# Kernel tuning notes

Measured on AMD Instinct MI355X. Metric: run time of the kernel, lower is better.

Reference implementation:

```python
import jax, jax.numpy as jnp
import numpy as np

N_U, N_I, E, D = 100000, 50000, 1600000, 128


def setup_inputs() -> dict:
    key = jax.random.key(0)
    ks = jax.random.split(key, 24)
    inp = {
        "x_user": jax.random.normal(ks[0], (N_U, D), jnp.float32),
        "x_item": jax.random.normal(ks[1], (N_I, D), jnp.float32),
        "follows_src": jax.random.randint(ks[2], (E,), 0, N_U, jnp.int32),
        "follows_dst": jax.random.randint(ks[3], (E,), 0, N_U, jnp.int32),
        "rates_src": jax.random.randint(ks[4], (E,), 0, N_U, jnp.int32),
        "rates_dst": jax.random.randint(ks[5], (E,), 0, N_I, jnp.int32),
        "rev_src": jax.random.randint(ks[6], (E,), 0, N_I, jnp.int32),
        "rev_dst": jax.random.randint(ks[7], (E,), 0, N_U, jnp.int32),
    }
    scale = 1.0 / np.sqrt(D)
    wnames = ["W1_follows", "W1_rates", "W1_rev", "W2_follows", "W2_rates", "W2_rev"]
    for i, name in enumerate(wnames):
        inp[name] = jax.random.normal(ks[8 + i], (D, D), jnp.float32) * scale
    bnames = ["b1_follows", "b1_rates", "b1_rev", "b2_follows", "b2_rates", "b2_rev"]
    for i, name in enumerate(bnames):
        inp[name] = jax.random.normal(ks[14 + i], (D,), jnp.float32) * 0.02
    return inp


def _gcn_conv(x_src, src, dst, n_src, n_dst, W, b):
    """Degree-normalized GCN conv on a (possibly bipartite) relation."""
    ones = jnp.ones(src.shape, x_src.dtype)
    deg_s = jax.ops.segment_sum(ones, src, num_segments=n_src)
    deg_d = jax.ops.segment_sum(ones, dst, num_segments=n_dst)
    inv_s = jnp.where(deg_s > 0, 1.0 / jnp.sqrt(deg_s), 0.0)
    inv_d = jnp.where(deg_d > 0, 1.0 / jnp.sqrt(deg_d), 0.0)
    h = x_src @ W                                   # [n_src, out]
    norm = inv_s[src] * inv_d[dst]                  # [E]
    msg = h[src] * norm[:, None]                    # gather + scale
    out = jax.ops.segment_sum(msg, dst, num_segments=n_dst)  # scatter-add
    return out + b


def reference(x_user, x_item, follows_src, follows_dst, rates_src, rates_dst,
              rev_src, rev_dst, W1_follows, b1_follows, W1_rates, b1_rates,
              W1_rev, b1_rev, W2_follows, b2_follows, W2_rates, b2_rates,
              W2_rev, b2_rev):
    # Layer 1: HeteroConv with aggr='mean' over relations sharing dst type
    u = (_gcn_conv(x_user, follows_src, follows_dst, N_U, N_U, W1_follows, b1_follows)
         + _gcn_conv(x_item, rev_src, rev_dst, N_I, N_U, W1_rev, b1_rev)) * 0.5
    it = _gcn_conv(x_user, rates_src, rates_dst, N_U, N_I, W1_rates, b1_rates)
    u = jax.nn.relu(u)
    it = jax.nn.relu(it)
    # Layer 2 (final layer: no relu)
    u2 = (_gcn_conv(u, follows_src, follows_dst, N_U, N_U, W2_follows, b2_follows)
          + _gcn_conv(it, rev_src, rev_dst, N_I, N_U, W2_rev, b2_rev)) * 0.5
    i2 = _gcn_conv(u, rates_src, rates_dst, N_U, N_I, W2_rates, b2_rates)
    # concat node-type outputs into a single array: [N_U + N_I, D]
    return jnp.concatenate([u2, i2], axis=0)
```

## Files before the change

kernel.cpp:

```cpp
#include <hip/hip_runtime.h>
#include <math.h>

static constexpr int NU    = 100000;
static constexpr int NI    = 50000;
static constexpr int NEDGE = 1600000;
static constexpr int DIM   = 128;

static constexpr int CB  = 768;
static constexpr int GF  = (NU + 127) / 128;
static constexpr int GV  = (NI + 127) / 128;
static constexpr int FB  = 512;
static constexpr int AGU = (NU + 3) / 4;
static constexpr int AGI = (NI + 3) / 4;

__device__ __forceinline__ void count_rel(const int* __restrict__ src, const int* __restrict__ dst,
                                          int* __restrict__ deg_s, int* __restrict__ deg_d,
                                          int* __restrict__ rank, int blk, int nblk) {
  const int nchunk = NEDGE / 4;
  const int stride = nblk * 256;
  for (int c = blk * 256 + threadIdx.x; c < nchunk; c += stride) {
    int4 s = ((const int4*)src)[c];
    int4 d = ((const int4*)dst)[c];
    atomicAdd(&deg_s[s.x], 1);
    atomicAdd(&deg_s[s.y], 1);
    atomicAdd(&deg_s[s.z], 1);
    atomicAdd(&deg_s[s.w], 1);
    int4 r;
    r.x = atomicAdd(&deg_d[d.x], 1);
    r.y = atomicAdd(&deg_d[d.y], 1);
    r.z = atomicAdd(&deg_d[d.z], 1);
    r.w = atomicAdd(&deg_d[d.w], 1);
    ((int4*)rank)[c] = r;
  }
}

__device__ __forceinline__ void fill_rel(const int* __restrict__ src, const int* __restrict__ dst,
                                         const int* __restrict__ rank, const int* __restrict__ rp,
                                         int* __restrict__ csr, int blk, int nblk) {
  const int nchunk = NEDGE / 4;
  const int stride = nblk * 256;
  for (int c = blk * 256 + threadIdx.x; c < nchunk; c += stride) {
    int4 s = ((const int4*)src)[c];
    int4 d = ((const int4*)dst)[c];
    int4 r = ((const int4*)rank)[c];
    csr[rp[d.x] + r.x] = s.x;
    csr[rp[d.y] + r.y] = s.y;
    csr[rp[d.z] + r.z] = s.z;
    csr[rp[d.w] + r.w] = s.w;
  }
}

__device__ __forceinline__ void gemm_body(const float* __restrict__ A, const float* __restrict__ W,
                                          float* __restrict__ C, int M, int blk) {
  static __shared__ float As[16][132];
  static __shared__ float Bs[16][128];
  const int tid = threadIdx.x;
  const int tx = tid & 15, ty = tid >> 4;
  const int row0 = blk * 128;
  float acc[8][8];
#pragma unroll
  for (int r = 0; r < 8; ++r)
#pragma unroll
    for (int c = 0; c < 8; ++c) acc[r][c] = 0.f;

  for (int kk = 0; kk < DIM; kk += 16) {
#pragma unroll
    for (int p = 0; p < 2; ++p) {
      int r = (tid >> 2) + p * 64;
      int kc = (tid & 3) * 4;
      float4 a = make_float4(0.f, 0.f, 0.f, 0.f);
      int row = row0 + r;
      if (row < M) a = *(const float4*)(A + (size_t)row * DIM + kk + kc);
      As[kc + 0][r] = a.x; As[kc + 1][r] = a.y; As[kc + 2][r] = a.z; As[kc + 3][r] = a.w;
    }
    {
      const float4* srcp = (const float4*)(W + kk * DIM);
      float4* dstp = (float4*)(&Bs[0][0]);
      dstp[tid]       = srcp[tid];
      dstp[tid + 256] = srcp[tid + 256];
    }
    __syncthreads();
#pragma unroll
    for (int k = 0; k < 16; ++k) {
      float a[8], b[8];
      *(float4*)&a[0] = *(const float4*)&As[k][ty * 8];
      *(float4*)&a[4] = *(const float4*)&As[k][ty * 8 + 4];
      *(float4*)&b[0] = *(const float4*)&Bs[k][tx * 8];
      *(float4*)&b[4] = *(const float4*)&Bs[k][tx * 8 + 4];
#pragma unroll
      for (int r = 0; r < 8; ++r)
#pragma unroll
        for (int c = 0; c < 8; ++c) acc[r][c] += a[r] * b[c];
    }
    __syncthreads();
  }
#pragma unroll
  for (int r = 0; r < 8; ++r) {
    int row = row0 + ty * 8 + r;
    if (row < M) {
      float4* cp = (float4*)(C + (size_t)row * DIM + tx * 8);
      cp[0] = make_float4(acc[r][0], acc[r][1], acc[r][2], acc[r][3]);
      cp[1] = make_float4(acc[r][4], acc[r][5], acc[r][6], acc[r][7]);
    }
  }
}

template <int MODE, bool RELU>
__device__ __forceinline__ void agg_rows(const float* __restrict__ h, const int* __restrict__ rp,
                                         const int* __restrict__ csr, const float* __restrict__ inv_s,
                                         const float* __restrict__ inv_d, float* __restrict__ out,
                                         int n_dst, float scale, const float* __restrict__ b1,
                                         const float* __restrict__ b2, int blk) {
  const int lane = threadIdx.x & 63;
  const int row = blk * 4 + (threadIdx.x >> 6);
  if (row >= n_dst) return;
  const int e0 = rp[row], e1 = rp[row + 1];
  float ax = 0.f, ay = 0.f;
  for (int base = e0; base < e1; base += 64) {
    const int rem = e1 - base;
    const int m = rem < 64 ? rem : 64;
    int s_l = 0; float w_l = 0.f;
    if (lane < m) { s_l = csr[base + lane]; w_l = inv_s[s_l]; }
    int j = 0;
    for (; j + 3 < m; j += 4) {
      int s0 = __shfl(s_l, j), s1 = __shfl(s_l, j + 1), s2 = __shfl(s_l, j + 2), s3 = __shfl(s_l, j + 3);
      float w0 = __shfl(w_l, j), w1 = __shfl(w_l, j + 1), w2 = __shfl(w_l, j + 2), w3 = __shfl(w_l, j + 3);
      float2 v0 = ((const float2*)(h + (size_t)s0 * DIM))[lane];
      float2 v1 = ((const float2*)(h + (size_t)s1 * DIM))[lane];
      float2 v2 = ((const float2*)(h + (size_t)s2 * DIM))[lane];
      float2 v3 = ((const float2*)(h + (size_t)s3 * DIM))[lane];
      ax += w0 * v0.x + w1 * v1.x + w2 * v2.x + w3 * v3.x;
      ay += w0 * v0.y + w1 * v1.y + w2 * v2.y + w3 * v3.y;
    }
    for (; j < m; ++j) {
      int s0 = __shfl(s_l, j); float w0 = __shfl(w_l, j);
      float2 v0 = ((const float2*)(h + (size_t)s0 * DIM))[lane];
      ax += w0 * v0.x; ay += w0 * v0.y;
    }
  }
  const float invd = inv_d[row];
  float rx = ax * invd, ry = ay * invd;
  float2* op = (float2*)(out + (size_t)row * DIM);
  if (MODE == 0) {
    op[lane] = make_float2(rx, ry);
  } else {
    float bx = 0.f, by = 0.f;
    if (b1) { float2 b = ((const float2*)b1)[lane]; bx += b.x; by += b.y; }
    if (b2) { float2 b = ((const float2*)b2)[lane]; bx += b.x; by += b.y; }
    float px = 0.f, py = 0.f;
    if (MODE == 1) { float2 p = op[lane]; px = p.x; py = p.y; }
    float vx = scale * (px + rx + bx), vy = scale * (py + ry + by);
    if (RELU) { vx = fmaxf(vx, 0.f); vy = fmaxf(vy, 0.f); }
    op[lane] = make_float2(vx, vy);
  }
}

__device__ void scan_body(const int* __restrict__ deg, int n, int* __restrict__ rp) {
  static __shared__ int wsum[16];
  static __shared__ int carry_s;
  const int tid = threadIdx.x, lane = tid & 63, wid = tid >> 6;
  if (tid == 0) carry_s = 0;
  __syncthreads();
  for (int base = 0; base < n; base += 4096) {
    int i0 = base + tid * 4;
    int v0 = 0, v1 = 0, v2 = 0, v3 = 0;
    if (i0 + 3 < n) {
      int4 t = *(const int4*)(deg + i0);
      v0 = t.x; v1 = t.y; v2 = t.z; v3 = t.w;
    } else {
      if (i0     < n) v0 = deg[i0];
      if (i0 + 1 < n) v1 = deg[i0 + 1];
      if (i0 + 2 < n) v2 = deg[i0 + 2];
    }
    int s0 = v0, s1 = s0 + v1, s2 = s1 + v2, s3 = s2 + v3;
    int tot = s3;
    int x = tot;
#pragma unroll
    for (int d2 = 1; d2 < 64; d2 <<= 1) { int y = __shfl_up(x, d2); if (lane >= d2) x += y; }
    if (lane == 63) wsum[wid] = x;
    __syncthreads();
    if (wid == 0) {
      int s = (lane < 16) ? wsum[lane] : 0;
#pragma unroll
      for (int d2 = 1; d2 < 16; d2 <<= 1) { int y = __shfl_up(s, d2); if (lane >= d2) s += y; }
      if (lane < 16) wsum[lane] = s;
    }
    __syncthreads();
    int carry = carry_s;
    int woff = (wid > 0) ? wsum[wid - 1] : 0;
    int base_excl = carry + woff + (x - tot);
    if (i0     < n) rp[i0]     = base_excl;
    if (i0 + 1 < n) rp[i0 + 1] = base_excl + s0;
    if (i0 + 2 < n) rp[i0 + 2] = base_excl + s1;
    if (i0 + 3 < n) rp[i0 + 3] = base_excl + s2;
    __syncthreads();
    if (tid == 0) carry_s = carry + wsum[15];
    __syncthreads();
  }
  if (tid == 0) rp[n] = carry_s;
}


__global__ __launch_bounds__(256) void k1_kernel(
    const int* f_src, const int* f_dst, int* deg_fs, int* deg_fd, int* rank_f,
    const int* r_src, const int* r_dst, int* deg_rs, int* deg_rd, int* rank_r,
    const int* v_src, const int* v_dst, int* deg_vs, int* deg_vd, int* rank_v,
    const float* x_user, const float* x_item,
    const float* W1f, const float* W1v, const float* W1r,
    float* h_f, float* h_v, float* h_r) {
  int b = blockIdx.x;
  if (b < CB) {
    count_rel(f_src, f_dst, deg_fs, deg_fd, rank_f, b, CB);
    count_rel(r_src, r_dst, deg_rs, deg_rd, rank_r, b, CB);
    count_rel(v_src, v_dst, deg_vs, deg_vd, rank_v, b, CB);
  } else if (b < CB + GF) {
    gemm_body(x_user, W1f, h_f, NU, b - CB);
  } else if (b < CB + GF + GV) {
    gemm_body(x_item, W1v, h_v, NI, b - CB - GF);
  } else {
    gemm_body(x_user, W1r, h_r, NU, b - CB - GF - GV);
  }
}

__global__ __launch_bounds__(1024) void scan3_kernel(const int* deg_fd, int* rp_f,
                                                     const int* deg_rd, int* rp_r,
                                                     const int* deg_vd, int* rp_v) {
  if (blockIdx.x == 0)      scan_body(deg_fd, NU, rp_f);
  else if (blockIdx.x == 1) scan_body(deg_rd, NI, rp_r);
  else                      scan_body(deg_vd, NU, rp_v);
}

__global__ void inv_sqrt_kernel(int* __restrict__ p, int n) {
  int i = blockIdx.x * blockDim.x + threadIdx.x;
  if (i < n) {
    int v = p[i];
    float f = (v > 0) ? (1.0f / sqrtf((float)v)) : 0.0f;
    p[i] = __float_as_int(f);
  }
}

__global__ __launch_bounds__(256) void fill_one_kernel(const int* src, const int* dst,
                                                       const int* rank, const int* rp, int* csr) {
  fill_rel(src, dst, rank, rp, csr, blockIdx.x, gridDim.x);
}

__global__ __launch_bounds__(256) void fill_vr_kernel(
    const int* v_src, const int* v_dst, const int* rank_v, const int* rp_v, int* csr_v,
    const int* r_src, const int* r_dst, const int* rank_r, const int* rp_r, int* csr_r) {
  int b = blockIdx.x;
  if (b < FB) fill_rel(v_src, v_dst, rank_v, rp_v, csr_v, b, FB);
  else        fill_rel(r_src, r_dst, rank_r, rp_r, csr_r, b - FB, FB);
}

__global__ __launch_bounds__(256) void k4_kernel(
    const int* v_src, const int* v_dst, const int* rank_v, const int* rp_v, int* csr_v,
    const int* r_src, const int* r_dst, const int* rank_r, const int* rp_r, int* csr_r,
    const float* h_f, const int* rp_f, const int* csr_f,
    const float* inv_fs, const float* inv_fd, float* u) {
  int b = blockIdx.x;
  if (b < FB)          fill_rel(v_src, v_dst, rank_v, rp_v, csr_v, b, FB);
  else if (b < 2 * FB) fill_rel(r_src, r_dst, rank_r, rp_r, csr_r, b - FB, FB);
  else agg_rows<0, false>(h_f, rp_f, csr_f, inv_fs, inv_fd, u, NU, 1.0f, nullptr, nullptr, b - 2 * FB);
}

__global__ __launch_bounds__(256) void k5_kernel(
    const float* h_v, const int* rp_v, const int* csr_v, const float* inv_vs, const float* inv_vd,
    float* u, const float* b1f, const float* b1v,
    const float* h_r, const int* rp_r, const int* csr_r, const float* inv_rs, const float* inv_rd,
    float* it, const float* b1r) {
  int b = blockIdx.x;
  if (b < AGU) agg_rows<1, true>(h_v, rp_v, csr_v, inv_vs, inv_vd, u, NU, 0.5f, b1f, b1v, b);
  else         agg_rows<2, true>(h_r, rp_r, csr_r, inv_rs, inv_rd, it, NI, 1.0f, b1r, nullptr, b - AGU);
}

__global__ __launch_bounds__(256) void gemm_one_kernel(const float* A, const float* W, float* C, int M) {
  gemm_body(A, W, C, M, blockIdx.x);
}

__global__ __launch_bounds__(256) void k7_kernel(
    const float* it, const float* W2v, float* h_v,
    const float* u,  const float* W2r, float* h_r,
    const float* h_f, const int* rp_f, const int* csr_f,
    const float* inv_fs, const float* inv_fd, float* out_u) {
  int b = blockIdx.x;
  if (b < GV)           gemm_body(it, W2v, h_v, NI, b);
  else if (b < GV + GF) gemm_body(u, W2r, h_r, NU, b - GV);
  else agg_rows<0, false>(h_f, rp_f, csr_f, inv_fs, inv_fd, out_u, NU, 1.0f, nullptr, nullptr, b - GV - GF);
}

__global__ __launch_bounds__(256) void k8_kernel(
    const float* h_v, const int* rp_v, const int* csr_v, const float* inv_vs, const float* inv_vd,
    float* out_u, const float* b2f, const float* b2v,
    const float* h_r, const int* rp_r, const int* csr_r, const float* inv_rs, const float* inv_rd,
    float* out_i, const float* b2r) {
  int b = blockIdx.x;
  if (b < AGU) agg_rows<1, false>(h_v, rp_v, csr_v, inv_vs, inv_vd, out_u, NU, 0.5f, b2f, b2v, b);
  else         agg_rows<2, false>(h_r, rp_r, csr_r, inv_rs, inv_rd, out_i, NI, 1.0f, b2r, nullptr, b - AGU);
}

template <int MODE, bool RELU>
__global__ __launch_bounds__(256) void agg_kernel(const float* h, const int* rp, const int* csr,
                                                  const float* inv_s, const float* inv_d,
                                                  float* out, int n_dst, float scale,
                                                  const float* b1, const float* b2) {
  agg_rows<MODE, RELU>(h, rp, csr, inv_s, inv_d, out, n_dst, scale, b1, b2, blockIdx.x);
}

extern "C" void kernel_launch(void* const* d_in, const int* in_sizes, int n_in,
                              void* d_out, int out_size, void* d_ws, size_t ws_size,
                              hipStream_t stream) {
  const float* x_user = (const float*)d_in[0];
  const float* x_item = (const float*)d_in[1];
  const int* f_src = (const int*)d_in[2];
  const int* f_dst = (const int*)d_in[3];
  const int* r_src = (const int*)d_in[4];
  const int* r_dst = (const int*)d_in[5];
  const int* v_src = (const int*)d_in[6];
  const int* v_dst = (const int*)d_in[7];
  const float* W1f = (const float*)d_in[8];
  const float* W1r = (const float*)d_in[9];
  const float* W1v = (const float*)d_in[10];
  const float* W2f = (const float*)d_in[11];
  const float* W2r = (const float*)d_in[12];
  const float* W2v = (const float*)d_in[13];
  const float* b1f = (const float*)d_in[14];
  const float* b1r = (const float*)d_in[15];
  const float* b1v = (const float*)d_in[16];
  const float* b2f = (const float*)d_in[17];
  const float* b2r = (const float*)d_in[18];
  const float* b2v = (const float*)d_in[19];
  (void)in_sizes; (void)n_in; (void)out_size;

  char* ws = (char*)d_ws;
  size_t off = 0;
  auto alloc = [&](size_t bytes) {
    size_t o = off;
    off = (off + bytes + 511) & ~(size_t)511;
    return o;
  };
  size_t o_deg = alloc(4ull * (4 * NU + 2 * NI));
  size_t o_rpf = alloc(4ull * (NU + 1));
  size_t o_rpr = alloc(4ull * (NI + 1));
  size_t o_rpv = alloc(4ull * (NU + 1));
  size_t o_csf = alloc(4ull * NEDGE);
  size_t o_csr = alloc(4ull * NEDGE);
  size_t o_csv = alloc(4ull * NEDGE);
  size_t o_it  = alloc(4ull * NI * DIM);
  size_t o_hf  = alloc(4ull * NU * DIM);
  size_t o_u   = alloc(4ull * NU * DIM);
  size_t small_need = off + 512;
  size_t o_hv  = alloc(4ull * NI * DIM);
  size_t o_hr  = alloc(4ull * NU * DIM);
  size_t o_rkf = alloc(4ull * NEDGE);
  size_t o_rkr = alloc(4ull * NEDGE);
  size_t o_rkv = alloc(4ull * NEDGE);
  size_t big_need = off + 512;

  const bool big = (ws_size >= big_need);

  int* deg    = (int*)(ws + o_deg);
  int* deg_fs = deg;
  int* deg_fd = deg + NU;
  int* deg_rs = deg + 2 * NU;
  int* deg_rd = deg + 3 * NU;
  int* deg_vs = deg + 3 * NU + NI;
  int* deg_vd = deg + 3 * NU + 2 * NI;

  int* rp_f = (int*)(ws + o_rpf);
  int* rp_r = (int*)(ws + o_rpr);
  int* rp_v = (int*)(ws + o_rpv);
  int* csr_f = (int*)(ws + o_csf);
  int* csr_r = (int*)(ws + o_csr);
  int* csr_v = (int*)(ws + o_csv);
  float* it  = (float*)(ws + o_it);
  float* h_f = (float*)(ws + o_hf);
  float* u   = (float*)(ws + o_u);
  float* h_v = big ? (float*)(ws + o_hv) : h_f;
  float* h_r = big ? (float*)(ws + o_hr) : h_f;
  int* rank_f = big ? (int*)(ws + o_rkf) : (int*)(ws + o_u);
  int* rank_r = big ? (int*)(ws + o_rkr) : (int*)(ws + o_u) + NEDGE;
  int* rank_v = big ? (int*)(ws + o_rkv) : (int*)(ws + o_u) + 2 * NEDGE;
  (void)small_need;

  float* out_u = (float*)d_out;
  float* out_i = out_u + (size_t)NU * DIM;

  const float* inv_fs = (const float*)deg_fs;
  const float* inv_fd = (const float*)deg_fd;
  const float* inv_rs = (const float*)deg_rs;
  const float* inv_rd = (const float*)deg_rd;
  const float* inv_vs = (const float*)deg_vs;
  const float* inv_vd = (const float*)deg_vd;

  hipMemsetAsync(deg, 0, 4ull * (4 * NU + 2 * NI), stream);

  if (big) {
    k1_kernel<<<CB + GF + GV + GF, 256, 0, stream>>>(
        f_src, f_dst, deg_fs, deg_fd, rank_f,
        r_src, r_dst, deg_rs, deg_rd, rank_r,
        v_src, v_dst, deg_vs, deg_vd, rank_v,
        x_user, x_item, W1f, W1v, W1r, h_f, h_v, h_r);
    scan3_kernel<<<3, 1024, 0, stream>>>(deg_fd, rp_f, deg_rd, rp_r, deg_vd, rp_v);
    inv_sqrt_kernel<<<(4 * NU + 2 * NI + 1023) / 1024, 1024, 0, stream>>>(deg, 4 * NU + 2 * NI);
    fill_one_kernel<<<FB, 256, 0, stream>>>(f_src, f_dst, rank_f, rp_f, csr_f);
    k4_kernel<<<2 * FB + AGU, 256, 0, stream>>>(
        v_src, v_dst, rank_v, rp_v, csr_v,
        r_src, r_dst, rank_r, rp_r, csr_r,
        h_f, rp_f, csr_f, inv_fs, inv_fd, u);
    k5_kernel<<<AGU + AGI, 256, 0, stream>>>(
        h_v, rp_v, csr_v, inv_vs, inv_vd, u, b1f, b1v,
        h_r, rp_r, csr_r, inv_rs, inv_rd, it, b1r);
    gemm_one_kernel<<<GF, 256, 0, stream>>>(u, W2f, h_f, NU);
    k7_kernel<<<GV + GF + AGU, 256, 0, stream>>>(
        it, W2v, h_v, u, W2r, h_r,
        h_f, rp_f, csr_f, inv_fs, inv_fd, out_u);
    k8_kernel<<<AGU + AGI, 256, 0, stream>>>(
        h_v, rp_v, csr_v, inv_vs, inv_vd, out_u, b2f, b2v,
        h_r, rp_r, csr_r, inv_rs, inv_rd, out_i, b2r);
  } else {
    k1_kernel<<<CB, 256, 0, stream>>>(
        f_src, f_dst, deg_fs, deg_fd, rank_f,
        r_src, r_dst, deg_rs, deg_rd, rank_r,
        v_src, v_dst, deg_vs, deg_vd, rank_v,
        x_user, x_item, W1f, W1v, W1r, h_f, h_v, h_r);
    scan3_kernel<<<3, 1024, 0, stream>>>(deg_fd, rp_f, deg_rd, rp_r, deg_vd, rp_v);
    inv_sqrt_kernel<<<(4 * NU + 2 * NI + 1023) / 1024, 1024, 0, stream>>>(deg, 4 * NU + 2 * NI);
    fill_one_kernel<<<FB, 256, 0, stream>>>(f_src, f_dst, rank_f, rp_f, csr_f);
    fill_vr_kernel<<<2 * FB, 256, 0, stream>>>(
        v_src, v_dst, rank_v, rp_v, csr_v,
        r_src, r_dst, rank_r, rp_r, csr_r);
    gemm_one_kernel<<<GF, 256, 0, stream>>>(x_user, W1f, h_f, NU);
    agg_kernel<0, false><<<AGU, 256, 0, stream>>>(h_f, rp_f, csr_f, inv_fs, inv_fd, u, NU, 1.0f, nullptr, nullptr);
    gemm_one_kernel<<<GV, 256, 0, stream>>>(x_item, W1v, h_f, NI);
    agg_kernel<1, true><<<AGU, 256, 0, stream>>>(h_f, rp_v, csr_v, inv_vs, inv_vd, u, NU, 0.5f, b1f, b1v);
    gemm_one_kernel<<<GF, 256, 0, stream>>>(x_user, W1r, h_f, NU);
    agg_kernel<2, true><<<AGI, 256, 0, stream>>>(h_f, rp_r, csr_r, inv_rs, inv_rd, it, NI, 1.0f, b1r, nullptr);
    gemm_one_kernel<<<GF, 256, 0, stream>>>(u, W2f, h_f, NU);
    agg_kernel<0, false><<<AGU, 256, 0, stream>>>(h_f, rp_f, csr_f, inv_fs, inv_fd, out_u, NU, 1.0f, nullptr, nullptr);
    gemm_one_kernel<<<GV, 256, 0, stream>>>(it, W2v, h_f, NI);
    agg_kernel<1, false><<<AGU, 256, 0, stream>>>(h_f, rp_v, csr_v, inv_vs, inv_vd, out_u, NU, 0.5f, b2f, b2v);
    gemm_one_kernel<<<GF, 256, 0, stream>>>(u, W2r, h_f, NU);
    agg_kernel<2, false><<<AGI, 256, 0, stream>>>(h_f, rp_r, csr_r, inv_rs, inv_rd, out_i, NI, 1.0f, b2r, nullptr);
  }
}
```

Measured before the change: 1.945 ms.

## Retune layer-1 fused kernel, add 64-row GEMM tiles, widen aggregation gathers

The layer-1 GEMM blocks inside k1 now use a smaller 64-row tile, which doubles the GEMM block count, and the degree-counting block count and occupancy bound are raised. The edge aggregation now has each half-wave process a different edge with float4 loads, and the two halves are combined by a cross-half shuffle, which should give more memory-level parallelism per wave. The fill kernel grid is enlarged, and the fallback path splits the fused fill into separate launches. The smaller GEMM tile reuses the weights less per row, and the shuffle reduction adds a little extra work.

```diff
diff --git a/kernel.cpp b/kernel.cpp
--- a/kernel.cpp
+++ b/kernel.cpp
@@ -6,12 +6,14 @@
 static constexpr int NEDGE = 1600000;
 static constexpr int DIM   = 128;
 
-static constexpr int CB  = 768;
-static constexpr int GF  = (NU + 127) / 128;
-static constexpr int GV  = (NI + 127) / 128;
-static constexpr int FB  = 512;
-static constexpr int AGU = (NU + 3) / 4;
-static constexpr int AGI = (NI + 3) / 4;
+static constexpr int CB   = 1792;
+static constexpr int GF   = (NU + 127) / 128;
+static constexpr int GV   = (NI + 127) / 128;
+static constexpr int GF2  = (NU + 63) / 64;
+static constexpr int GV2  = (NI + 63) / 64;
+static constexpr int FB   = 512;
+static constexpr int AGU  = (NU + 3) / 4;
+static constexpr int AGI  = (NI + 3) / 4;
 
 __device__ __forceinline__ void count_rel(const int* __restrict__ src, const int* __restrict__ dst,
                                           int* __restrict__ deg_s, int* __restrict__ deg_d,
@@ -105,6 +107,59 @@
   }
 }
 
+__device__ __forceinline__ void gemm64_body(const float* __restrict__ A, const float* __restrict__ W,
+                                            float* __restrict__ C, int M, int blk) {
+  static __shared__ float As6[16][68];
+  static __shared__ float Bs6[16][128];
+  const int tid = threadIdx.x;
+  const int tx = tid & 15, ty = tid >> 4;
+  const int row0 = blk * 64;
+  float acc[4][8];
+#pragma unroll
+  for (int r = 0; r < 4; ++r)
+#pragma unroll
+    for (int c = 0; c < 8; ++c) acc[r][c] = 0.f;
+
+  for (int kk = 0; kk < DIM; kk += 16) {
+    {
+      int r = tid >> 2;
+      int kc = (tid & 3) * 4;
+      float4 a = make_float4(0.f, 0.f, 0.f, 0.f);
+      int row = row0 + r;
+      if (row < M) a = *(const float4*)(A + (size_t)row * DIM + kk + kc);
+      As6[kc + 0][r] = a.x; As6[kc + 1][r] = a.y; As6[kc + 2][r] = a.z; As6[kc + 3][r] = a.w;
+    }
+    {
+      const float4* srcp = (const float4*)(W + kk * DIM);
+      float4* dstp = (float4*)(&Bs6[0][0]);
+      dstp[tid]       = srcp[tid];
+      dstp[tid + 256] = srcp[tid + 256];
+    }
+    __syncthreads();
+#pragma unroll
+    for (int k = 0; k < 16; ++k) {
+      float a[4], b[8];
+      *(float4*)&a[0] = *(const float4*)&As6[k][ty * 4];
+      *(float4*)&b[0] = *(const float4*)&Bs6[k][tx * 8];
+      *(float4*)&b[4] = *(const float4*)&Bs6[k][tx * 8 + 4];
+#pragma unroll
+      for (int r = 0; r < 4; ++r)
+#pragma unroll
+        for (int c = 0; c < 8; ++c) acc[r][c] += a[r] * b[c];
+    }
+    __syncthreads();
+  }
+#pragma unroll
+  for (int r = 0; r < 4; ++r) {
+    int row = row0 + ty * 4 + r;
+    if (row < M) {
+      float4* cp = (float4*)(C + (size_t)row * DIM + tx * 8);
+      cp[0] = make_float4(acc[r][0], acc[r][1], acc[r][2], acc[r][3]);
+      cp[1] = make_float4(acc[r][4], acc[r][5], acc[r][6], acc[r][7]);
+    }
+  }
+}
+
 template <int MODE, bool RELU>
 __device__ __forceinline__ void agg_rows(const float* __restrict__ h, const int* __restrict__ rp,
                                          const int* __restrict__ csr, const float* __restrict__ inv_s,
@@ -112,46 +167,71 @@
                                          int n_dst, float scale, const float* __restrict__ b1,
                                          const float* __restrict__ b2, int blk) {
   const int lane = threadIdx.x & 63;
+  const int half = lane >> 5;
+  const int sl   = lane & 31;
   const int row = blk * 4 + (threadIdx.x >> 6);
   if (row >= n_dst) return;
   const int e0 = rp[row], e1 = rp[row + 1];
-  float ax = 0.f, ay = 0.f;
+  float4 acc = make_float4(0.f, 0.f, 0.f, 0.f);
   for (int base = e0; base < e1; base += 64) {
     const int rem = e1 - base;
     const int m = rem < 64 ? rem : 64;
     int s_l = 0; float w_l = 0.f;
     if (lane < m) { s_l = csr[base + lane]; w_l = inv_s[s_l]; }
     int j = 0;
-    for (; j + 3 < m; j += 4) {
-      int s0 = __shfl(s_l, j), s1 = __shfl(s_l, j + 1), s2 = __shfl(s_l, j + 2), s3 = __shfl(s_l, j + 3);
-      float w0 = __shfl(w_l, j), w1 = __shfl(w_l, j + 1), w2 = __shfl(w_l, j + 2), w3 = __shfl(w_l, j + 3);
-      float2 v0 = ((const float2*)(h + (size_t)s0 * DIM))[lane];
-      float2 v1 = ((const float2*)(h + (size_t)s1 * DIM))[lane];
-      float2 v2 = ((const float2*)(h + (size_t)s2 * DIM))[lane];
-      float2 v3 = ((const float2*)(h + (size_t)s3 * DIM))[lane];
-      ax += w0 * v0.x + w1 * v1.x + w2 * v2.x + w3 * v3.x;
-      ay += w0 * v0.y + w1 * v1.y + w2 * v2.y + w3 * v3.y;
-    }
-    for (; j < m; ++j) {
-      int s0 = __shfl(s_l, j); float w0 = __shfl(w_l, j);
-      float2 v0 = ((const float2*)(h + (size_t)s0 * DIM))[lane];
-      ax += w0 * v0.x; ay += w0 * v0.y;
-    }
-  }
-  const float invd = inv_d[row];
-  float rx = ax * invd, ry = ay * invd;
-  float2* op = (float2*)(out + (size_t)row * DIM);
-  if (MODE == 0) {
-    op[lane] = make_float2(rx, ry);
-  } else {
-    float bx = 0.f, by = 0.f;
-    if (b1) { float2 b = ((const float2*)b1)[lane]; bx += b.x; by += b.y; }
-    if (b2) { float2 b = ((const float2*)b2)[lane]; bx += b.x; by += b.y; }
-    float px = 0.f, py = 0.f;
-    if (MODE == 1) { float2 p = op[lane]; px = p.x; py = p.y; }
-    float vx = scale * (px + rx + bx), vy = scale * (py + ry + by);
-    if (RELU) { vx = fmaxf(vx, 0.f); vy = fmaxf(vy, 0.f); }
-    op[lane] = make_float2(vx, vy);
+    for (; j + 8 <= m; j += 8) {
+      const int eb = j + half * 4;
+      int s0 = __shfl(s_l, eb),     s1 = __shfl(s_l, eb + 1);
+      int s2 = __shfl(s_l, eb + 2), s3 = __shfl(s_l, eb + 3);
+      float w0 = __shfl(w_l, eb),     w1 = __shfl(w_l, eb + 1);
+      float w2 = __shfl(w_l, eb + 2), w3 = __shfl(w_l, eb + 3);
+      float4 v0 = ((const float4*)(h + (size_t)s0 * DIM))[sl];
+      float4 v1 = ((const float4*)(h + (size_t)s1 * DIM))[sl];
+      float4 v2 = ((const float4*)(h + (size_t)s2 * DIM))[sl];
+      float4 v3 = ((const float4*)(h + (size_t)s3 * DIM))[sl];
+      acc.x += w0 * v0.x + w1 * v1.x + w2 * v2.x + w3 * v3.x;
+      acc.y += w0 * v0.y + w1 * v1.y + w2 * v2.y + w3 * v3.y;
+      acc.z += w0 * v0.z + w1 * v1.z + w2 * v2.z + w3 * v3.z;
+      acc.w += w0 * v0.w + w1 * v1.w + w2 * v2.w + w3 * v3.w;
+    }
+    for (; j < m; j += 2) {
+      const int e = j + half;
+      int s = __shfl(s_l, e);
+      float w = __shfl(w_l, e);
+      float4 v = ((const float4*)(h + (size_t)s * DIM))[sl];
+      acc.x += w * v.x; acc.y += w * v.y; acc.z += w * v.z; acc.w += w * v.w;
+    }
+  }
+  float4 o;
+  o.x = __shfl(acc.x, lane ^ 32);
+  o.y = __shfl(acc.y, lane ^ 32);
+  o.z = __shfl(acc.z, lane ^ 32);
+  o.w = __shfl(acc.w, lane ^ 32);
+  acc.x += o.x; acc.y += o.y; acc.z += o.z; acc.w += o.w;
+
+  if (half == 0) {
+    const float invd = inv_d[row];
+    float4 r = make_float4(acc.x * invd, acc.y * invd, acc.z * invd, acc.w * invd);
+    float4* op4 = (float4*)(out + (size_t)row * DIM);
+    if (MODE == 0) {
+      op4[sl] = r;
+    } else {
+      float4 bv = make_float4(0.f, 0.f, 0.f, 0.f);
+      if (b1) { float4 b = ((const float4*)b1)[sl]; bv.x += b.x; bv.y += b.y; bv.z += b.z; bv.w += b.w; }
+      if (b2) { float4 b = ((const float4*)b2)[sl]; bv.x += b.x; bv.y += b.y; bv.z += b.z; bv.w += b.w; }
+      float4 p = make_float4(0.f, 0.f, 0.f, 0.f);
+      if (MODE == 1) p = op4[sl];
+      float4 v;
+      v.x = scale * (p.x + r.x + bv.x);
+      v.y = scale * (p.y + r.y + bv.y);
+      v.z = scale * (p.z + r.z + bv.z);
+      v.w = scale * (p.w + r.w + bv.w);
+      if (RELU) {
+        v.x = fmaxf(v.x, 0.f); v.y = fmaxf(v.y, 0.f);
+        v.z = fmaxf(v.z, 0.f); v.w = fmaxf(v.w, 0.f);
+      }
+      op4[sl] = v;
+    }
   }
 }
 
@@ -201,7 +281,7 @@
 }
 
 
-__global__ __launch_bounds__(256) void k1_kernel(
+__global__ __launch_bounds__(256, 8) void k1_kernel(
     const int* f_src, const int* f_dst, int* deg_fs, int* deg_fd, int* rank_f,
     const int* r_src, const int* r_dst, int* deg_rs, int* deg_rd, int* rank_r,
     const int* v_src, const int* v_dst, int* deg_vs, int* deg_vd, int* rank_v,
@@ -213,12 +293,12 @@
     count_rel(f_src, f_dst, deg_fs, deg_fd, rank_f, b, CB);
     count_rel(r_src, r_dst, deg_rs, deg_rd, rank_r, b, CB);
     count_rel(v_src, v_dst, deg_vs, deg_vd, rank_v, b, CB);
-  } else if (b < CB + GF) {
-    gemm_body(x_user, W1f, h_f, NU, b - CB);
-  } else if (b < CB + GF + GV) {
-    gemm_body(x_item, W1v, h_v, NI, b - CB - GF);
+  } else if (b < CB + GF2) {
+    gemm64_body(x_user, W1f, h_f, NU, b - CB);
+  } else if (b < CB + GF2 + GV2) {
+    gemm64_body(x_item, W1v, h_v, NI, b - CB - GF2);
   } else {
-    gemm_body(x_user, W1r, h_r, NU, b - CB - GF - GV);
+    gemm64_body(x_user, W1r, h_r, NU, b - CB - GF2 - GV2);
   }
 }
 
@@ -242,14 +322,6 @@
 __global__ __launch_bounds__(256) void fill_one_kernel(const int* src, const int* dst,
                                                        const int* rank, const int* rp, int* csr) {
   fill_rel(src, dst, rank, rp, csr, blockIdx.x, gridDim.x);
-}
-
-__global__ __launch_bounds__(256) void fill_vr_kernel(
-    const int* v_src, const int* v_dst, const int* rank_v, const int* rp_v, int* csr_v,
-    const int* r_src, const int* r_dst, const int* rank_r, const int* rp_r, int* csr_r) {
-  int b = blockIdx.x;
-  if (b < FB) fill_rel(v_src, v_dst, rank_v, rp_v, csr_v, b, FB);
-  else        fill_rel(r_src, r_dst, rank_r, rp_r, csr_r, b - FB, FB);
 }
 
 __global__ __launch_bounds__(256) void k4_kernel(
@@ -348,7 +420,6 @@
   size_t o_it  = alloc(4ull * NI * DIM);
   size_t o_hf  = alloc(4ull * NU * DIM);
   size_t o_u   = alloc(4ull * NU * DIM);
-  size_t small_need = off + 512;
   size_t o_hv  = alloc(4ull * NI * DIM);
   size_t o_hr  = alloc(4ull * NU * DIM);
   size_t o_rkf = alloc(4ull * NEDGE);
@@ -380,7 +451,6 @@
   int* rank_f = big ? (int*)(ws + o_rkf) : (int*)(ws + o_u);
   int* rank_r = big ? (int*)(ws + o_rkr) : (int*)(ws + o_u) + NEDGE;
   int* rank_v = big ? (int*)(ws + o_rkv) : (int*)(ws + o_u) + 2 * NEDGE;
-  (void)small_need;
 
   float* out_u = (float*)d_out;
   float* out_i = out_u + (size_t)NU * DIM;
@@ -395,14 +465,14 @@
   hipMemsetAsync(deg, 0, 4ull * (4 * NU + 2 * NI), stream);
 
   if (big) {
-    k1_kernel<<<CB + GF + GV + GF, 256, 0, stream>>>(
+    k1_kernel<<<CB + GF2 + GV2 + GF2, 256, 0, stream>>>(
         f_src, f_dst, deg_fs, deg_fd, rank_f,
         r_src, r_dst, deg_rs, deg_rd, rank_r,
         v_src, v_dst, deg_vs, deg_vd, rank_v,
         x_user, x_item, W1f, W1v, W1r, h_f, h_v, h_r);
     scan3_kernel<<<3, 1024, 0, stream>>>(deg_fd, rp_f, deg_rd, rp_r, deg_vd, rp_v);
     inv_sqrt_kernel<<<(4 * NU + 2 * NI + 1023) / 1024, 1024, 0, stream>>>(deg, 4 * NU + 2 * NI);
-    fill_one_kernel<<<FB, 256, 0, stream>>>(f_src, f_dst, rank_f, rp_f, csr_f);
+    fill_one_kernel<<<1024, 256, 0, stream>>>(f_src, f_dst, rank_f, rp_f, csr_f);
     k4_kernel<<<2 * FB + AGU, 256, 0, stream>>>(
         v_src, v_dst, rank_v, rp_v, csr_v,
         r_src, r_dst, rank_r, rp_r, csr_r,
@@ -425,10 +495,9 @@
         x_user, x_item, W1f, W1v, W1r, h_f, h_v, h_r);
     scan3_kernel<<<3, 1024, 0, stream>>>(deg_fd, rp_f, deg_rd, rp_r, deg_vd, rp_v);
     inv_sqrt_kernel<<<(4 * NU + 2 * NI + 1023) / 1024, 1024, 0, stream>>>(deg, 4 * NU + 2 * NI);
-    fill_one_kernel<<<FB, 256, 0, stream>>>(f_src, f_dst, rank_f, rp_f, csr_f);
-    fill_vr_kernel<<<2 * FB, 256, 0, stream>>>(
-        v_src, v_dst, rank_v, rp_v, csr_v,
-        r_src, r_dst, rank_r, rp_r, csr_r);
+    fill_one_kernel<<<1024, 256, 0, stream>>>(f_src, f_dst, rank_f, rp_f, csr_f);
+    fill_one_kernel<<<1024, 256, 0, stream>>>(v_src, v_dst, rank_v, rp_v, csr_v);
+    fill_one_kernel<<<1024, 256, 0, stream>>>(r_src, r_dst, rank_r, rp_r, csr_r);
     gemm_one_kernel<<<GF, 256, 0, stream>>>(x_user, W1f, h_f, NU);
     agg_kernel<0, false><<<AGU, 256, 0, stream>>>(h_f, rp_f, csr_f, inv_fs, inv_fd, u, NU, 1.0f, nullptr, nullptr);
     gemm_one_kernel<<<GV, 256, 0, stream>>>(x_item, W1v, h_f, NI);
```

Measured after the change: 2.613 ms. 1.34x slower.
